# Optimization experiments

Hardware: AMD Instinct MI355X
Metric: run time of the kernel (lower is better)

Reference implementation:

```python
import jax, jax.numpy as jnp
import numpy as np

B, H, W, K, PAD = 1024, 28, 28, 3, 1


def conv3x3(x, w, b):
    out = jax.lax.conv_general_dilated(x, w, (1, 1), ((PAD, PAD), (PAD, PAD)),
                                       dimension_numbers=('NCHW', 'OIHW', 'NCHW'))
    return out + b[None, :, None, None]


def deform_conv2d(x, offset, w, b):
    # torchvision deform_conv2d semantics, stride=1, pad=1, dilation=1, groups=1
    Bn, Cin, Hh, Ww = x.shape
    Cout = w.shape[0]
    KK = K * K
    off = offset.reshape(Bn, KK, 2, Hh, Ww)
    dy, dx = off[:, :, 0], off[:, :, 1]                      # [B,KK,H,W]
    ky, kx = jnp.meshgrid(jnp.arange(K, dtype=x.dtype), jnp.arange(K, dtype=x.dtype), indexing='ij')
    py = dy + (jnp.arange(Hh, dtype=x.dtype) - PAD)[None, None, :, None] + ky.reshape(KK)[None, :, None, None]
    px = dx + (jnp.arange(Ww, dtype=x.dtype) - PAD)[None, None, None, :] + kx.reshape(KK)[None, :, None, None]
    y0 = jnp.floor(py); x0 = jnp.floor(px)
    wy1 = py - y0; wy0 = 1.0 - wy1
    wx1 = px - x0; wx0 = 1.0 - wx1
    xf = x.reshape(Bn, Cin, Hh * Ww)

    def gather(yi, xi):
        valid = (yi >= 0) & (yi < Hh) & (xi >= 0) & (xi < Ww)
        yc = jnp.clip(yi, 0, Hh - 1).astype(jnp.int32)
        xc = jnp.clip(xi, 0, Ww - 1).astype(jnp.int32)
        idx = (yc * Ww + xc).reshape(Bn, -1)                 # [B, KK*H*W]
        g = jnp.take_along_axis(xf, jnp.broadcast_to(idx[:, None, :], (Bn, Cin, idx.shape[1])), axis=2)
        return g.reshape(Bn, Cin, KK, Hh, Ww) * valid.astype(x.dtype)[:, None]

    sampled = (gather(y0, x0) * (wy0 * wx0)[:, None]
               + gather(y0, x0 + 1) * (wy0 * wx1)[:, None]
               + gather(y0 + 1, x0) * (wy1 * wx0)[:, None]
               + gather(y0 + 1, x0 + 1) * (wy1 * wx1)[:, None])  # [B,Cin,KK,H,W]
    out = jnp.einsum('bkhw,ok->bohw', sampled.reshape(Bn, Cin * KK, Hh, Ww),
                     w.reshape(Cout, Cin * KK))
    return out + b[None, :, None, None]


def adaptive_avg_pool_14(x):
    Bn, C, Hh, Ww = x.shape
    f = Hh // 14
    return x.reshape(Bn, C, 14, f, 14, f).mean(axis=(3, 5))


def setup_inputs() -> dict:
    key = jax.random.key(0)
    ks = jax.random.split(key, 14)
    d = {}
    d['x'] = jax.random.normal(ks[0], (B, 1, H, W), dtype=jnp.float32)
    # offset conv 1: Conv2d(1, 18, 3, pad=1)
    d['ow1'] = jax.random.normal(ks[1], (18, 1, 3, 3), dtype=jnp.float32) * 0.1
    d['ob1'] = jnp.zeros((18,), jnp.float32)
    d['w1'] = jax.random.normal(ks[2], (32, 1, 3, 3), dtype=jnp.float32) * 0.01
    d['b1'] = jnp.zeros((32,), jnp.float32)
    # offset conv 2: Conv2d(32, 18, 3, pad=1)
    d['ow2'] = jax.random.normal(ks[3], (18, 32, 3, 3), dtype=jnp.float32) * 0.05
    d['ob2'] = jnp.zeros((18,), jnp.float32)
    d['w2'] = jax.random.normal(ks[4], (64, 32, 3, 3), dtype=jnp.float32) * 0.01
    d['b2'] = jnp.zeros((64,), jnp.float32)
    d['fw1'] = jax.random.normal(ks[5], (128, 64 * 14 * 14), dtype=jnp.float32) * 0.01
    d['fb1'] = jnp.zeros((128,), jnp.float32)
    d['fw2'] = jax.random.normal(ks[6], (10, 128), dtype=jnp.float32) * 0.05
    d['fb2'] = jnp.zeros((10,), jnp.float32)
    return d


def reference(x, ow1, ob1, w1, b1, ow2, ob2, w2, b2, fw1, fb1, fw2, fb2):
    # block1 + relu + pool 28->14
    h = deform_conv2d(x, conv3x3(x, ow1, ob1), w1, b1)
    h = adaptive_avg_pool_14(jax.nn.relu(h))
    # block2 + relu + pool 14->14 (identity)
    h = deform_conv2d(h, conv3x3(h, ow2, ob2), w2, b2)
    h = adaptive_avg_pool_14(jax.nn.relu(h))
    h = h.reshape(h.shape[0], -1)
    # classifier (ExcitationDropout is identity in eval mode)
    h = jax.nn.relu(h @ fw1.T + fb1)
    return h @ fw2.T + fb2
```

## Files before the change

### kernel.cpp

```cpp
#include <hip/hip_runtime.h>

#define NB 1024
#define TOTAL1 (NB*196)
#define SPS 200

#define WS_H1   0
#define WS_H2   6422528
#define WS_PART 19267584
#define WS_W1T  23461888
#define WS_OW1T 23462176
#define WS_W2T  23462338
#define WS_OW2T 23480770

__global__ __launch_bounds__(256) void prep(const float* __restrict__ w1,
                                            const float* __restrict__ ow1,
                                            const float* __restrict__ w2,
                                            const float* __restrict__ ow2,
                                            float* __restrict__ ws) {
  int i = blockIdx.x * 256 + threadIdx.x;
  if (i < 288)   { int co = i / 9,  kk = i % 9;   ws[WS_W1T  + kk * 32 + co] = w1[i]; }
  if (i < 162)   { int c  = i / 9,  j  = i % 9;   ws[WS_OW1T + j  * 18 + c ] = ow1[i]; }
  if (i < 18432) { int co = i / 288, k = i % 288; ws[WS_W2T  + k  * 64 + co] = w2[i]; }
  if (i < 5184)  { int c  = i / 288, k = i % 288; ws[WS_OW2T + k  * 18 + c ] = ow2[i]; }
}

__global__ __launch_bounds__(256, 2) void stage1(const float* __restrict__ x,
                                                 const float* __restrict__ ob1,
                                                 const float* __restrict__ b1,
                                                 const float* __restrict__ ws,
                                                 float* __restrict__ h1) {
  __shared__ float ximg[3 * 784];
  const float* __restrict__ w1t  = ws + WS_W1T;
  const float* __restrict__ ow1t = ws + WS_OW1T;
  int tid = threadIdx.x;
  int g0 = blockIdx.x * 256;
  int bfirst = g0 / 196;
  for (int idx = tid; idx < 3 * 784; idx += 256) {
    int img = idx / 784;
    int b = bfirst + img;
    ximg[idx] = (b < NB) ? x[b * 784 + (idx - img * 784)] : 0.f;
  }
  __syncthreads();
  int g = g0 + tid;
  if (g >= TOTAL1) return;
  int b = g / 196, p = g - b * 196;
  const float* im = ximg + (b - bfirst) * 784;
  int oy = p / 14, ox = p - (p / 14) * 14;

  float pooled[32];
#pragma unroll
  for (int co = 0; co < 32; ++co) pooled[co] = 0.f;

  for (int sub = 0; sub < 4; ++sub) {
    int y  = 2 * oy + (sub >> 1);
    int ix = 2 * ox + (sub & 1);
    float patch[9];
#pragma unroll
    for (int j = 0; j < 9; ++j) {
      int yy = y + j / 3 - 1, xc = ix + j % 3 - 1;
      bool ok = (yy >= 0) & (yy < 28) & (xc >= 0) & (xc < 28);
      patch[j] = ok ? im[yy * 28 + xc] : 0.f;
    }
    float off[18];
#pragma unroll
    for (int c = 0; c < 18; ++c) off[c] = ob1[c];
#pragma unroll
    for (int j = 0; j < 9; ++j) {
      float v = patch[j];
#pragma unroll
      for (int c = 0; c < 18; ++c) off[c] = fmaf(v, ow1t[j * 18 + c], off[c]);
    }
    float a[32];
#pragma unroll
    for (int co = 0; co < 32; ++co) a[co] = b1[co];
#pragma unroll
    for (int kk = 0; kk < 9; ++kk) {
      float py = (float)(y - 1 + kk / 3) + off[2 * kk];
      float px = (float)(ix - 1 + kk % 3) + off[2 * kk + 1];
      float y0f = floorf(py), x0f = floorf(px);
      float wy1 = py - y0f, wx1 = px - x0f;
      float wy0 = 1.f - wy1, wx0 = 1.f - wx1;
      int y0 = (int)y0f, x0 = (int)x0f;
      int y1 = y0 + 1, x1 = x0 + 1;
      bool vy0 = (y0 >= 0) & (y0 < 28), vy1 = (y1 >= 0) & (y1 < 28);
      bool vx0 = (x0 >= 0) & (x0 < 28), vx1 = (x1 >= 0) & (x1 < 28);
      float W00 = (vy0 & vx0) ? wy0 * wx0 : 0.f;
      float W01 = (vy0 & vx1) ? wy0 * wx1 : 0.f;
      float W10 = (vy1 & vx0) ? wy1 * wx0 : 0.f;
      float W11 = (vy1 & vx1) ? wy1 * wx1 : 0.f;
      int yc0 = min(max(y0, 0), 27), yc1 = min(max(y1, 0), 27);
      int xc0 = min(max(x0, 0), 27), xc1 = min(max(x1, 0), 27);
      float s = im[yc0 * 28 + xc0] * W00 + im[yc0 * 28 + xc1] * W01 +
                im[yc1 * 28 + xc0] * W10 + im[yc1 * 28 + xc1] * W11;
#pragma unroll
      for (int co = 0; co < 32; ++co) a[co] = fmaf(s, w1t[kk * 32 + co], a[co]);
    }
#pragma unroll
    for (int co = 0; co < 32; ++co) pooled[co] += fmaxf(a[co], 0.f);
  }
#pragma unroll
  for (int co = 0; co < 32; ++co) h1[b * 6272 + co * 196 + p] = pooled[co] * 0.25f;
}

__global__ __launch_bounds__(256, 3) void stage2(const float* __restrict__ h1,
                                                 const float* __restrict__ ob2,
                                                 const float* __restrict__ b2,
                                                 const float* __restrict__ ws,
                                                 float* __restrict__ h2) {
  __shared__ float imgT[196 * 32];
  __shared__ float Sbuf[32 * SPS + 8];
  __shared__ float offT[2 * 208];
  const float* __restrict__ w2t  = ws + WS_W2T;
  const float* __restrict__ ow2t = ws + WS_OW2T;
  int tid = threadIdx.x;
  int b = blockIdx.x;

  for (int e = tid; e < 6272; e += 256) {
    int ci = e / 196, p = e - ci * 196;
    imgT[p * 32 + ((ci + 4 * p) & 31)] = h1[b * 6272 + e];
  }
  if (tid < 128) Sbuf[(tid >> 2) * SPS + 196 + (tid & 3)] = 0.f;
  if (tid < 8)   Sbuf[32 * SPS + tid] = 0.f;

  int pp = tid;
  int spy = pp / 14, spx = pp - (pp / 14) * 14;

  int oc  = tid % 18;
  int opg = tid / 18;
  int op0 = opg * 16;
  bool oact = (tid < 234);
  float oacc[16];
#pragma unroll
  for (int i = 0; i < 16; ++i) oacc[i] = 0.f;

  for (int j = 0; j < 9; ++j) {
    __syncthreads();
    if (pp < 196) {
      int yy = spy + j / 3 - 1, xx = spx + j % 3 - 1;
      bool ok = (yy >= 0) & (yy < 14) & (xx >= 0) & (xx < 14);
      int idx = ok ? (yy * 14 + xx) : 0;
      const float* src = imgT + idx * 32;
      int rot = (4 * idx) & 31;
#pragma unroll
      for (int cg = 0; cg < 8; ++cg) {
        float4 v;
        if (ok) v = *(const float4*)(src + ((cg * 4 + rot) & 31));
        else    v = make_float4(0.f, 0.f, 0.f, 0.f);
        Sbuf[(cg * 4 + 0) * SPS + pp] = v.x;
        Sbuf[(cg * 4 + 1) * SPS + pp] = v.y;
        Sbuf[(cg * 4 + 2) * SPS + pp] = v.z;
        Sbuf[(cg * 4 + 3) * SPS + pp] = v.w;
      }
    }
    __syncthreads();
    if (oact) {
      float wv[32];
#pragma unroll
      for (int ci2 = 0; ci2 < 32; ++ci2) wv[ci2] = ow2t[(ci2 * 9 + j) * 18 + oc];
      for (int ci2 = 0; ci2 < 32; ++ci2) {
        const float* srow = Sbuf + ci2 * SPS + op0;
        float w = wv[ci2];
#pragma unroll
        for (int t = 0; t < 4; ++t) {
          float4 s = *(const float4*)(srow + 4 * t);
          oacc[4 * t + 0] = fmaf(w, s.x, oacc[4 * t + 0]);
          oacc[4 * t + 1] = fmaf(w, s.y, oacc[4 * t + 1]);
          oacc[4 * t + 2] = fmaf(w, s.z, oacc[4 * t + 2]);
          oacc[4 * t + 3] = fmaf(w, s.w, oacc[4 * t + 3]);
        }
      }
    }
  }

  int cog = tid & 15, pg = tid >> 4;
  int co0 = cog * 4;
  int p0 = pg * 16;
  bool gact = (pg < 13);
  float acc[4][16];
  {
    float4 bb = *(const float4*)(b2 + co0);
    float bj[4] = {bb.x, bb.y, bb.z, bb.w};
#pragma unroll
    for (int jj = 0; jj < 4; ++jj)
#pragma unroll
      for (int i = 0; i < 16; ++i) acc[jj][i] = bj[jj];
  }
  float myob = oact ? ob2[oc] : 0.f;

  for (int kk = 0; kk < 9; ++kk) {
    __syncthreads();
    if (oact && (oc >> 1) == kk) {
      float* dst = offT + (oc & 1) * 208 + op0;
#pragma unroll
      for (int i = 0; i < 16; ++i) dst[i] = oacc[i] + myob;
    }
    __syncthreads();
    if (pp < 196) {
      float dyv = offT[pp];
      float dxv = offT[208 + pp];
      float pyv = (float)(spy - 1 + kk / 3) + dyv;
      float pxv = (float)(spx - 1 + kk % 3) + dxv;
      float y0f = floorf(pyv), x0f = floorf(pxv);
      float wy1 = pyv - y0f, wx1 = pxv - x0f;
      float wy0 = 1.f - wy1, wx0 = 1.f - wx1;
      int y0 = (int)y0f, x0 = (int)x0f;
      int y1 = y0 + 1, x1 = x0 + 1;
      bool vy0 = (y0 >= 0) & (y0 < 14), vy1 = (y1 >= 0) & (y1 < 14);
      bool vx0 = (x0 >= 0) & (x0 < 14), vx1 = (x1 >= 0) & (x1 < 14);
      float W00 = (vy0 & vx0) ? wy0 * wx0 : 0.f;
      float W01 = (vy0 & vx1) ? wy0 * wx1 : 0.f;
      float W10 = (vy1 & vx0) ? wy1 * wx0 : 0.f;
      float W11 = (vy1 & vx1) ? wy1 * wx1 : 0.f;
      int yc0 = min(max(y0, 0), 13), yc1 = min(max(y1, 0), 13);
      int xc0 = min(max(x0, 0), 13), xc1 = min(max(x1, 0), 13);
      int i00 = yc0 * 14 + xc0, i01 = yc0 * 14 + xc1;
      int i10 = yc1 * 14 + xc0, i11 = yc1 * 14 + xc1;
      const float* s00 = imgT + i00 * 32; int r00 = (4 * i00) & 31;
      const float* s01 = imgT + i01 * 32; int r01 = (4 * i01) & 31;
      const float* s10 = imgT + i10 * 32; int r10 = (4 * i10) & 31;
      const float* s11 = imgT + i11 * 32; int r11 = (4 * i11) & 31;
#pragma unroll
      for (int cg = 0; cg < 8; ++cg) {
        float4 a0 = *(const float4*)(s00 + ((cg * 4 + r00) & 31));
        float4 a1 = *(const float4*)(s01 + ((cg * 4 + r01) & 31));
        float4 a2 = *(const float4*)(s10 + ((cg * 4 + r10) & 31));
        float4 a3 = *(const float4*)(s11 + ((cg * 4 + r11) & 31));
        Sbuf[(cg * 4 + 0) * SPS + pp] = fmaf(W00, a0.x, fmaf(W01, a1.x, fmaf(W10, a2.x, W11 * a3.x)));
        Sbuf[(cg * 4 + 1) * SPS + pp] = fmaf(W00, a0.y, fmaf(W01, a1.y, fmaf(W10, a2.y, W11 * a3.y)));
        Sbuf[(cg * 4 + 2) * SPS + pp] = fmaf(W00, a0.z, fmaf(W01, a1.z, fmaf(W10, a2.z, W11 * a3.z)));
        Sbuf[(cg * 4 + 3) * SPS + pp] = fmaf(W00, a0.w, fmaf(W01, a1.w, fmaf(W10, a2.w, W11 * a3.w)));
      }
    }
    __syncthreads();
    if (gact) {
      for (int cb = 0; cb < 32; cb += 4) {
        float4 w[4];
#pragma unroll
        for (int u = 0; u < 4; ++u)
          w[u] = *(const float4*)(w2t + ((cb + u) * 9 + kk) * 64 + co0);
#pragma unroll
        for (int u = 0; u < 4; ++u) {
          const float* srow = Sbuf + (cb + u) * SPS + p0;
          float4 s0 = *(const float4*)(srow);
          float4 s1 = *(const float4*)(srow + 4);
          float4 s2 = *(const float4*)(srow + 8);
          float4 s3 = *(const float4*)(srow + 12);
          float sv[16] = {s0.x, s0.y, s0.z, s0.w, s1.x, s1.y, s1.z, s1.w,
                          s2.x, s2.y, s2.z, s2.w, s3.x, s3.y, s3.z, s3.w};
          float wj[4] = {w[u].x, w[u].y, w[u].z, w[u].w};
#pragma unroll
          for (int jj = 0; jj < 4; ++jj)
#pragma unroll
            for (int i = 0; i < 16; ++i)
              acc[jj][i] = fmaf(wj[jj], sv[i], acc[jj][i]);
        }
      }
    }
  }

  if (gact) {
    float* __restrict__ orow = h2 + b * 12544 + co0 * 196 + p0;
#pragma unroll
    for (int jj = 0; jj < 4; ++jj) {
#pragma unroll
      for (int t = 0; t < 4; ++t) {
        if (p0 + 4 * t < 196) {
          float4 v;
          v.x = fmaxf(acc[jj][4 * t + 0], 0.f);
          v.y = fmaxf(acc[jj][4 * t + 1], 0.f);
          v.z = fmaxf(acc[jj][4 * t + 2], 0.f);
          v.w = fmaxf(acc[jj][4 * t + 3], 0.f);
          *(float4*)(orow + jj * 196 + 4 * t) = v;
        }
      }
    }
  }
}

__global__ __launch_bounds__(256, 3) void fc1(const float* __restrict__ h2,
                                              const float* __restrict__ fw1,
                                              float* __restrict__ part) {
  __shared__ float a_s[56 * 72];
  __shared__ float b_s[56 * 132];
  int tid = threadIdx.x;
  int rb = (blockIdx.x & 15) * 64;
  int ks = blockIdx.x >> 4;
  int kbase = ks * 392;
  int c0 = (tid & 31) * 4;
  int r0 = (tid >> 5) * 8;

  float acc[8][4];
#pragma unroll
  for (int i = 0; i < 8; ++i)
#pragma unroll
    for (int j = 0; j < 4; ++j) acc[i][j] = 0.f;

  for (int ch = 0; ch < 7; ++ch) {
    int kb = kbase + ch * 56;
    __syncthreads();
#pragma unroll
    for (int t = 0; t < 4; ++t) {
      int idx = t * 256 + tid;
      if (idx < 896) {
        int k4 = idx % 14, r = idx / 14;
        float4 v = *(const float4*)&h2[(rb + r) * 12544 + kb + k4 * 4];
        a_s[(k4 * 4 + 0) * 72 + r] = v.x;
        a_s[(k4 * 4 + 1) * 72 + r] = v.y;
        a_s[(k4 * 4 + 2) * 72 + r] = v.z;
        a_s[(k4 * 4 + 3) * 72 + r] = v.w;
      }
    }
#pragma unroll
    for (int t = 0; t < 7; ++t) {
      int idx = t * 256 + tid;
      int k4 = idx % 14, c = idx / 14;
      float4 v = *(const float4*)&fw1[c * 12544 + kb + k4 * 4];
      b_s[(k4 * 4 + 0) * 132 + c] = v.x;
      b_s[(k4 * 4 + 1) * 132 + c] = v.y;
      b_s[(k4 * 4 + 2) * 132 + c] = v.z;
      b_s[(k4 * 4 + 3) * 132 + c] = v.w;
    }
    __syncthreads();
    for (int k = 0; k < 56; ++k) {
      float4 bv = *(const float4*)&b_s[k * 132 + c0];
      float4 av0 = *(const float4*)&a_s[k * 72 + r0];
      float4 av1 = *(const float4*)&a_s[k * 72 + r0 + 4];
      float av[8] = {av0.x, av0.y, av0.z, av0.w, av1.x, av1.y, av1.z, av1.w};
      float bj[4] = {bv.x, bv.y, bv.z, bv.w};
#pragma unroll
      for (int i = 0; i < 8; ++i)
#pragma unroll
        for (int j = 0; j < 4; ++j) acc[i][j] = fmaf(av[i], bj[j], acc[i][j]);
    }
  }
#pragma unroll
  for (int i = 0; i < 8; ++i) {
    int r = rb + r0 + i;
#pragma unroll
    for (int j = 0; j < 4; ++j)
      part[(ks * 1024 + r) * 128 + c0 + j] = acc[i][j];
  }
}

__global__ __launch_bounds__(128) void fcfinal(const float* __restrict__ part,
                                               const float* __restrict__ fb1,
                                               const float* __restrict__ fw2,
                                               const float* __restrict__ fb2,
                                               float* __restrict__ out) {
  __shared__ float tbuf[128];
  int b = blockIdx.x, c = threadIdx.x;
  float s0 = 0.f, s1 = 0.f, s2 = 0.f, s3 = 0.f;
#pragma unroll
  for (int ks = 0; ks < 32; ks += 4) {
    s0 += part[((ks + 0) * 1024 + b) * 128 + c];
    s1 += part[((ks + 1) * 1024 + b) * 128 + c];
    s2 += part[((ks + 2) * 1024 + b) * 128 + c];
    s3 += part[((ks + 3) * 1024 + b) * 128 + c];
  }
  float s = fb1[c] + ((s0 + s1) + (s2 + s3));
  tbuf[c] = fmaxf(s, 0.f);
  __syncthreads();
  if (c < 10) {
    float v = fb2[c];
#pragma unroll
    for (int k = 0; k < 128; ++k) v = fmaf(tbuf[k], fw2[c * 128 + k], v);
    out[b * 10 + c] = v;
  }
}

extern "C" void kernel_launch(void* const* d_in, const int* in_sizes, int n_in,
                              void* d_out, int out_size, void* d_ws, size_t ws_size,
                              hipStream_t stream) {
  const float* x   = (const float*)d_in[0];
  const float* ow1 = (const float*)d_in[1];
  const float* ob1 = (const float*)d_in[2];
  const float* w1  = (const float*)d_in[3];
  const float* b1  = (const float*)d_in[4];
  const float* ow2 = (const float*)d_in[5];
  const float* ob2 = (const float*)d_in[6];
  const float* w2  = (const float*)d_in[7];
  const float* b2  = (const float*)d_in[8];
  const float* fw1 = (const float*)d_in[9];
  const float* fb1 = (const float*)d_in[10];
  const float* fw2 = (const float*)d_in[11];
  const float* fb2 = (const float*)d_in[12];
  float* ws  = (float*)d_ws;
  float* out = (float*)d_out;

  prep<<<72, 256, 0, stream>>>(w1, ow1, w2, ow2, ws);
  stage1<<<784, 256, 0, stream>>>(x, ob1, b1, ws, ws + WS_H1);
  stage2<<<NB, 256, 0, stream>>>(ws + WS_H1, ob2, b2, ws, ws + WS_H2);
  fc1<<<512, 256, 0, stream>>>(ws + WS_H2, fw1, ws + WS_PART);
  fcfinal<<<1024, 128, 0, stream>>>(ws + WS_PART, fb1, fw2, fb2, out);
}
```

Before: 385.0 us.

## Restructure stage2 deform GEMM to per-pixel 64-channel register accumulation

Stage2 now stores all 18 offset channels in shared memory once, after the offset convolution. The deformable conv then runs per pixel: each thread bilinearly samples its 32 input channels and accumulates all 64 output channels in registers, with weights read through uniform (scalar) loads. This removes the per-tap Sbuf staging round trip and its 18 barriers, and the offset convolution's Sbuf is halved by processing channels in two halves. The cost is a 64-float accumulator per thread, which raises register pressure and may reduce occupancy. The 60 idle threads (tid ≥ 196) also sit out the main GEMM.

Result: slower. 468.5 us (+21.7%).

```diff
diff --git a/kernel.cpp b/kernel.cpp
--- a/kernel.cpp
+++ b/kernel.cpp
@@ -108,8 +108,8 @@
                                                  const float* __restrict__ ws,
                                                  float* __restrict__ h2) {
   __shared__ float imgT[196 * 32];
-  __shared__ float Sbuf[32 * SPS + 8];
-  __shared__ float offT[2 * 208];
+  __shared__ float Sbuf[16 * SPS + 8];
+  __shared__ float offT18[18 * 208];
   const float* __restrict__ w2t  = ws + WS_W2T;
   const float* __restrict__ ow2t = ws + WS_OW2T;
   int tid = threadIdx.x;
@@ -119,11 +119,12 @@
     int ci = e / 196, p = e - ci * 196;
     imgT[p * 32 + ((ci + 4 * p) & 31)] = h1[b * 6272 + e];
   }
-  if (tid < 128) Sbuf[(tid >> 2) * SPS + 196 + (tid & 3)] = 0.f;
-  if (tid < 8)   Sbuf[32 * SPS + tid] = 0.f;
+  if (tid < 64) Sbuf[(tid >> 2) * SPS + 196 + (tid & 3)] = 0.f;
+  if (tid < 8)  Sbuf[16 * SPS + tid] = 0.f;
 
   int pp = tid;
   int spy = pp / 14, spx = pp - (pp / 14) * 14;
+  bool samp = (pp < 196);
 
   int oc  = tid % 18;
   int opg = tid / 18;
@@ -134,70 +135,63 @@
   for (int i = 0; i < 16; ++i) oacc[i] = 0.f;
 
   for (int j = 0; j < 9; ++j) {
-    __syncthreads();
-    if (pp < 196) {
-      int yy = spy + j / 3 - 1, xx = spx + j % 3 - 1;
-      bool ok = (yy >= 0) & (yy < 14) & (xx >= 0) & (xx < 14);
-      int idx = ok ? (yy * 14 + xx) : 0;
-      const float* src = imgT + idx * 32;
-      int rot = (4 * idx) & 31;
-#pragma unroll
-      for (int cg = 0; cg < 8; ++cg) {
-        float4 v;
-        if (ok) v = *(const float4*)(src + ((cg * 4 + rot) & 31));
-        else    v = make_float4(0.f, 0.f, 0.f, 0.f);
-        Sbuf[(cg * 4 + 0) * SPS + pp] = v.x;
-        Sbuf[(cg * 4 + 1) * SPS + pp] = v.y;
-        Sbuf[(cg * 4 + 2) * SPS + pp] = v.z;
-        Sbuf[(cg * 4 + 3) * SPS + pp] = v.w;
-      }
-    }
-    __syncthreads();
-    if (oact) {
-      float wv[32];
-#pragma unroll
-      for (int ci2 = 0; ci2 < 32; ++ci2) wv[ci2] = ow2t[(ci2 * 9 + j) * 18 + oc];
-      for (int ci2 = 0; ci2 < 32; ++ci2) {
-        const float* srow = Sbuf + ci2 * SPS + op0;
-        float w = wv[ci2];
-#pragma unroll
-        for (int t = 0; t < 4; ++t) {
-          float4 s = *(const float4*)(srow + 4 * t);
-          oacc[4 * t + 0] = fmaf(w, s.x, oacc[4 * t + 0]);
-          oacc[4 * t + 1] = fmaf(w, s.y, oacc[4 * t + 1]);
-          oacc[4 * t + 2] = fmaf(w, s.z, oacc[4 * t + 2]);
-          oacc[4 * t + 3] = fmaf(w, s.w, oacc[4 * t + 3]);
+    for (int h = 0; h < 2; ++h) {
+      __syncthreads();
+      if (samp) {
+        int yy = spy + j / 3 - 1, xx = spx + j % 3 - 1;
+        bool ok = (yy >= 0) & (yy < 14) & (xx >= 0) & (xx < 14);
+        int idx = ok ? (yy * 14 + xx) : 0;
+        const float* src = imgT + idx * 32;
+        int rot = (4 * idx) & 31;
+#pragma unroll
+        for (int cg = 0; cg < 4; ++cg) {
+          int cgg = h * 4 + cg;
+          float4 v;
+          if (ok) v = *(const float4*)(src + ((cgg * 4 + rot) & 31));
+          else    v = make_float4(0.f, 0.f, 0.f, 0.f);
+          Sbuf[(cg * 4 + 0) * SPS + pp] = v.x;
+          Sbuf[(cg * 4 + 1) * SPS + pp] = v.y;
+          Sbuf[(cg * 4 + 2) * SPS + pp] = v.z;
+          Sbuf[(cg * 4 + 3) * SPS + pp] = v.w;
         }
       }
-    }
-  }
-
-  int cog = tid & 15, pg = tid >> 4;
-  int co0 = cog * 4;
-  int p0 = pg * 16;
-  bool gact = (pg < 13);
-  float acc[4][16];
-  {
-    float4 bb = *(const float4*)(b2 + co0);
-    float bj[4] = {bb.x, bb.y, bb.z, bb.w};
-#pragma unroll
-    for (int jj = 0; jj < 4; ++jj)
-#pragma unroll
-      for (int i = 0; i < 16; ++i) acc[jj][i] = bj[jj];
-  }
-  float myob = oact ? ob2[oc] : 0.f;
-
-  for (int kk = 0; kk < 9; ++kk) {
-    __syncthreads();
-    if (oact && (oc >> 1) == kk) {
-      float* dst = offT + (oc & 1) * 208 + op0;
-#pragma unroll
-      for (int i = 0; i < 16; ++i) dst[i] = oacc[i] + myob;
-    }
-    __syncthreads();
-    if (pp < 196) {
-      float dyv = offT[pp];
-      float dxv = offT[208 + pp];
+      __syncthreads();
+      if (oact) {
+        float wv[16];
+#pragma unroll
+        for (int l = 0; l < 16; ++l) wv[l] = ow2t[((h * 16 + l) * 9 + j) * 18 + oc];
+        for (int l = 0; l < 16; ++l) {
+          const float* srow = Sbuf + l * SPS + op0;
+          float w = wv[l];
+#pragma unroll
+          for (int t = 0; t < 4; ++t) {
+            float4 s = *(const float4*)(srow + 4 * t);
+            oacc[4 * t + 0] = fmaf(w, s.x, oacc[4 * t + 0]);
+            oacc[4 * t + 1] = fmaf(w, s.y, oacc[4 * t + 1]);
+            oacc[4 * t + 2] = fmaf(w, s.z, oacc[4 * t + 2]);
+            oacc[4 * t + 3] = fmaf(w, s.w, oacc[4 * t + 3]);
+          }
+        }
+      }
+    }
+  }
+
+  if (oact) {
+    float bias = ob2[oc];
+    float* dst = offT18 + oc * 208 + op0;
+#pragma unroll
+    for (int i = 0; i < 16; ++i) dst[i] = oacc[i] + bias;
+  }
+  __syncthreads();
+
+  if (samp) {
+    float acc[64];
+#pragma unroll
+    for (int u = 0; u < 64; ++u) acc[u] = b2[u];
+
+    for (int kk = 0; kk < 9; ++kk) {
+      float dyv = offT18[(2 * kk) * 208 + pp];
+      float dxv = offT18[(2 * kk + 1) * 208 + pp];
       float pyv = (float)(spy - 1 + kk / 3) + dyv;
       float pxv = (float)(spx - 1 + kk % 3) + dxv;
       float y0f = floorf(pyv), x0f = floorf(pxv);
@@ -220,60 +214,31 @@
       const float* s10 = imgT + i10 * 32; int r10 = (4 * i10) & 31;
       const float* s11 = imgT + i11 * 32; int r11 = (4 * i11) & 31;
 #pragma unroll
-      for (int cg = 0; cg < 8; ++cg) {
-        float4 a0 = *(const float4*)(s00 + ((cg * 4 + r00) & 31));
-        float4 a1 = *(const float4*)(s01 + ((cg * 4 + r01) & 31));
-        float4 a2 = *(const float4*)(s10 + ((cg * 4 + r10) & 31));
-        float4 a3 = *(const float4*)(s11 + ((cg * 4 + r11) & 31));
-        Sbuf[(cg * 4 + 0) * SPS + pp] = fmaf(W00, a0.x, fmaf(W01, a1.x, fmaf(W10, a2.x, W11 * a3.x)));
-        Sbuf[(cg * 4 + 1) * SPS + pp] = fmaf(W00, a0.y, fmaf(W01, a1.y, fmaf(W10, a2.y, W11 * a3.y)));
-        Sbuf[(cg * 4 + 2) * SPS + pp] = fmaf(W00, a0.z, fmaf(W01, a1.z, fmaf(W10, a2.z, W11 * a3.z)));
-        Sbuf[(cg * 4 + 3) * SPS + pp] = fmaf(W00, a0.w, fmaf(W01, a1.w, fmaf(W10, a2.w, W11 * a3.w)));
-      }
-    }
-    __syncthreads();
-    if (gact) {
-      for (int cb = 0; cb < 32; cb += 4) {
-        float4 w[4];
-#pragma unroll
-        for (int u = 0; u < 4; ++u)
-          w[u] = *(const float4*)(w2t + ((cb + u) * 9 + kk) * 64 + co0);
+      for (int cq = 0; cq < 8; ++cq) {
+        float4 a0 = *(const float4*)(s00 + ((cq * 4 + r00) & 31));
+        float4 a1 = *(const float4*)(s01 + ((cq * 4 + r01) & 31));
+        float4 a2 = *(const float4*)(s10 + ((cq * 4 + r10) & 31));
+        float4 a3 = *(const float4*)(s11 + ((cq * 4 + r11) & 31));
+        float sv[4];
+        sv[0] = fmaf(W00, a0.x, fmaf(W01, a1.x, fmaf(W10, a2.x, W11 * a3.x)));
+        sv[1] = fmaf(W00, a0.y, fmaf(W01, a1.y, fmaf(W10, a2.y, W11 * a3.y)));
+        sv[2] = fmaf(W00, a0.z, fmaf(W01, a1.z, fmaf(W10, a2.z, W11 * a3.z)));
+        sv[3] = fmaf(W00, a0.w, fmaf(W01, a1.w, fmaf(W10, a2.w, W11 * a3.w)));
 #pragma unroll
         for (int u = 0; u < 4; ++u) {
-          const float* srow = Sbuf + (cb + u) * SPS + p0;
-          float4 s0 = *(const float4*)(srow);
-          float4 s1 = *(const float4*)(srow + 4);
-          float4 s2 = *(const float4*)(srow + 8);
-          float4 s3 = *(const float4*)(srow + 12);
-          float sv[16] = {s0.x, s0.y, s0.z, s0.w, s1.x, s1.y, s1.z, s1.w,
-                          s2.x, s2.y, s2.z, s2.w, s3.x, s3.y, s3.z, s3.w};
-          float wj[4] = {w[u].x, w[u].y, w[u].z, w[u].w};
-#pragma unroll
-          for (int jj = 0; jj < 4; ++jj)
-#pragma unroll
-            for (int i = 0; i < 16; ++i)
-              acc[jj][i] = fmaf(wj[jj], sv[i], acc[jj][i]);
+          const float* wr = w2t + ((cq * 4 + u) * 9 + kk) * 64;
+          float su = sv[u];
+#pragma unroll
+          for (int jj = 0; jj < 64; ++jj)
+            acc[jj] = fmaf(su, wr[jj], acc[jj]);
         }
       }
     }
-  }
-
-  if (gact) {
-    float* __restrict__ orow = h2 + b * 12544 + co0 * 196 + p0;
-#pragma unroll
-    for (int jj = 0; jj < 4; ++jj) {
-#pragma unroll
-      for (int t = 0; t < 4; ++t) {
-        if (p0 + 4 * t < 196) {
-          float4 v;
-          v.x = fmaxf(acc[jj][4 * t + 0], 0.f);
-          v.y = fmaxf(acc[jj][4 * t + 1], 0.f);
-          v.z = fmaxf(acc[jj][4 * t + 2], 0.f);
-          v.w = fmaxf(acc[jj][4 * t + 3], 0.f);
-          *(float4*)(orow + jj * 196 + 4 * t) = v;
-        }
-      }
-    }
+
+    int base = b * 12544 + pp;
+#pragma unroll
+    for (int u = 0; u < 64; ++u)
+      h2[base + u * 196] = fmaxf(acc[u], 0.f);
   }
 }
 
```
